# Kernel tuning notes

Measured on AMD Instinct MI355X. Metric: run time of the kernel, lower is better.

Reference implementation:

```python
import jax, jax.numpy as jnp
import numpy as np

ALPHA = 0.1
NUM_CLASSES = 10000
FEAT_DIM = 256
BATCH = 8192


def setup_inputs() -> dict:
    key = jax.random.key(0)
    k1, k2, k3 = jax.random.split(key, 3)
    feat = jax.random.normal(k1, (BATCH, FEAT_DIM), dtype=jnp.float32)
    label = jax.random.randint(k2, (BATCH,), 0, NUM_CLASSES, dtype=jnp.int64)
    # centers parameter, initialized ~ randn as in the torch constructor
    centers = jax.random.normal(k3, (NUM_CLASSES, FEAT_DIM), dtype=jnp.float32)
    return {"feat": feat, "label": label, "centers": centers}


def reference(feat, label, centers):
    B = feat.shape[0]
    # dist[b,c] = ||feat[b] - centers[c]||^2, computed in GEMM form:
    # ||f||^2 + ||c||^2 - 2 f.c  (same math as the broadcast diff^2 sum)
    f_sq = jnp.sum(feat * feat, axis=-1, keepdims=True)          # [B, 1]
    c_sq = jnp.sum(centers * centers, axis=-1)[None, :]          # [1, C]
    cross = jnp.einsum('bd,cd->bc', feat, centers)               # [B, C]
    dist = f_sq + c_sq - 2.0 * cross                             # [B, C]

    # one-hot margin scaling: y_onehot = alpha * onehot(label) + 1
    onehot = jax.nn.one_hot(label, NUM_CLASSES, dtype=dist.dtype)  # [B, C]
    margin_dist = dist * (onehot * ALPHA + 1.0)

    margin_logits = -0.5 * margin_dist
    logits = -0.5 * dist

    # likelihood: mean over batch of 0.5 * ||feat - centers[label]||^2
    cdiff = feat - centers[label]                                 # [B, D]
    likelihood = jnp.sum(cdiff * cdiff) / (2.0 * B)
    return (logits, margin_logits, likelihood)
```

## Files before the change

kernel.cpp:

```cpp
#include <hip/hip_runtime.h>
#include <hip/hip_bf16.h>


#define ALPHA_ 0.1f
constexpr int BATCH = 8192;
constexpr int NCLS  = 10000;
constexpr int FDIM  = 256;

typedef __attribute__((ext_vector_type(8))) short bf16x8;
typedef __attribute__((ext_vector_type(4))) float f32x4;

__device__ __forceinline__ unsigned short f2bf(float f) {
  unsigned int u = __float_as_uint(f);
  u += 0x7FFF + ((u >> 16) & 1);
  return (unsigned short)(u >> 16);
}

__global__ void prep_kernel(const float* __restrict__ feat,
                            const float* __restrict__ centers,
                            unsigned short* __restrict__ fbf,
                            unsigned short* __restrict__ cbf,
                            float* __restrict__ fsq,
                            float* __restrict__ csq) {
  int gw = (int)((blockIdx.x * blockDim.x + threadIdx.x) >> 6);
  int lane = threadIdx.x & 63;
  if (gw >= BATCH + NCLS) return;
  const float* src; unsigned short* dst; float* sq;
  if (gw < BATCH) {
    src = feat + (size_t)gw * FDIM; dst = fbf + (size_t)gw * FDIM; sq = fsq + gw;
  } else {
    int r = gw - BATCH;
    src = centers + (size_t)r * FDIM; dst = cbf + (size_t)r * FDIM; sq = csq + r;
  }
  float4 v = reinterpret_cast<const float4*>(src)[lane];
  ushort4 b;
  b.x = f2bf(v.x); b.y = f2bf(v.y); b.z = f2bf(v.z); b.w = f2bf(v.w);
  reinterpret_cast<ushort4*>(dst)[lane] = b;
  float s = v.x*v.x + v.y*v.y + v.z*v.z + v.w*v.w;
  #pragma unroll
  for (int off = 32; off >= 1; off >>= 1) s += __shfl_xor(s, off, 64);
  if (lane == 0) *sq = s;
}

#define BM 128
#define BN 128
#define BK 64
#define LDK 72

__global__ __launch_bounds__(512, 8)
void gemm_kernel(const unsigned short* __restrict__ fbf,
                 const unsigned short* __restrict__ cbf,
                 const float* __restrict__ fsq,
                 const float* __restrict__ csq,
                 const int* __restrict__ label,
                 float* __restrict__ out_logits,
                 float* __restrict__ out_margin) {
  __shared__ unsigned short As[BM * LDK];
  __shared__ unsigned short Bs[BN * LDK];

  const int NTN = (NCLS + BN - 1) / BN;
  const int NWG = (BATCH / BM) * NTN;

  int bid = blockIdx.x;
  int wg = (bid & 7) * (NWG >> 3) + (bid >> 3);
  int mt = wg / NTN;
  int nt = wg - mt * NTN;

  const int tid  = threadIdx.x;
  const int lane = tid & 63;
  const int wid  = tid >> 6;
  const int wr   = (wid >> 2) * 64;
  const int wc   = (wid & 3) * 32;

  f32x4 acc[4][2];
  #pragma unroll
  for (int i = 0; i < 4; i++)
    #pragma unroll
    for (int j = 0; j < 2; j++) acc[i][j] = (f32x4){0.f, 0.f, 0.f, 0.f};

  const int srow = tid >> 3;
  const int scol = (tid & 7) * 8;
  const size_t a_base = (size_t)(mt * BM) * FDIM;
  const int c0 = nt * BN;

  for (int kc = 0; kc < FDIM / BK; ++kc) {
    const int k0 = kc * BK;
    #pragma unroll
    for (int j = 0; j < 2; ++j) {
      int r = j * 64 + srow;
      bf16x8 v = *reinterpret_cast<const bf16x8*>(fbf + a_base + (size_t)r * FDIM + k0 + scol);
      *reinterpret_cast<bf16x8*>(&As[r * LDK + scol]) = v;
    }
    #pragma unroll
    for (int j = 0; j < 2; ++j) {
      int r = j * 64 + srow;
      int c = c0 + r;
      bf16x8 v = (bf16x8){0,0,0,0,0,0,0,0};
      if (c < NCLS) v = *reinterpret_cast<const bf16x8*>(cbf + (size_t)c * FDIM + k0 + scol);
      *reinterpret_cast<bf16x8*>(&Bs[r * LDK + scol]) = v;
    }
    __syncthreads();
    #pragma unroll
    for (int kk = 0; kk < BK / 32; ++kk) {
      const int kcol = kk * 32 + (lane >> 4) * 8;
      bf16x8 a[4], b[2];
      #pragma unroll
      for (int i = 0; i < 4; i++)
        a[i] = *reinterpret_cast<const bf16x8*>(&As[(wr + i * 16 + (lane & 15)) * LDK + kcol]);
      #pragma unroll
      for (int j = 0; j < 2; j++)
        b[j] = *reinterpret_cast<const bf16x8*>(&Bs[(wc + j * 16 + (lane & 15)) * LDK + kcol]);
      #pragma unroll
      for (int i = 0; i < 4; i++)
        #pragma unroll
        for (int j = 0; j < 2; j++)
          acc[i][j] = __builtin_amdgcn_mfma_f32_16x16x32_bf16(b[j], a[i], acc[i][j], 0, 0, 0);
    }
    __syncthreads();
  }

  const int mloc = wr + (lane & 15);
  const int nbase = wc + ((lane >> 4) << 2);
  #pragma unroll
  for (int i = 0; i < 4; i++) {
    int m = mt * BM + mloc + i * 16;
    float fs = fsq[m];
    int lb = label[m];
    size_t rowoff = (size_t)m * NCLS;
    #pragma unroll
    for (int j = 0; j < 2; j++) {
      int n0 = c0 + nbase + j * 16;
      if (n0 >= NCLS) continue;
      float4 cs = *reinterpret_cast<const float4*>(&csq[n0]);
      f32x4 v = acc[i][j];
      f32x4 lg;
      lg[0] = v[0] - 0.5f * (fs + cs.x);
      lg[1] = v[1] - 0.5f * (fs + cs.y);
      lg[2] = v[2] - 0.5f * (fs + cs.z);
      lg[3] = v[3] - 0.5f * (fs + cs.w);
      __builtin_nontemporal_store(lg, reinterpret_cast<f32x4*>(&out_logits[rowoff + n0]));
      f32x4 mg;
      mg[0] = (lb == n0    ) ? lg[0] * (1.0f + ALPHA_) : lg[0];
      mg[1] = (lb == n0 + 1) ? lg[1] * (1.0f + ALPHA_) : lg[1];
      mg[2] = (lb == n0 + 2) ? lg[2] * (1.0f + ALPHA_) : lg[2];
      mg[3] = (lb == n0 + 3) ? lg[3] * (1.0f + ALPHA_) : lg[3];
      __builtin_nontemporal_store(mg, reinterpret_cast<f32x4*>(&out_margin[rowoff + n0]));
    }
  }
}

__global__ void lik_partial_kernel(const float* __restrict__ feat,
                                   const int* __restrict__ label,
                                   const float* __restrict__ centers,
                                   float* __restrict__ partial) {
  int t = threadIdx.x;
  int b0 = blockIdx.x * 8;
  float acc = 0.f;
  #pragma unroll
  for (int i = 0; i < 8; i++) {
    int row = b0 + i;
    int lb = label[row];
    float d = feat[(size_t)row * FDIM + t] - centers[(size_t)lb * FDIM + t];
    acc += d * d;
  }
  #pragma unroll
  for (int off = 32; off >= 1; off >>= 1) acc += __shfl_xor(acc, off, 64);
  __shared__ float red[4];
  if ((t & 63) == 0) red[t >> 6] = acc;
  __syncthreads();
  if (t == 0) partial[blockIdx.x] = red[0] + red[1] + red[2] + red[3];
}

__global__ void lik_final_kernel(const float* __restrict__ partial,
                                 float* __restrict__ out) {
  int t = threadIdx.x;
  float v = partial[t] + partial[t + 256] + partial[t + 512] + partial[t + 768];
  #pragma unroll
  for (int off = 32; off >= 1; off >>= 1) v += __shfl_xor(v, off, 64);
  __shared__ float red[4];
  if ((t & 63) == 0) red[t >> 6] = v;
  __syncthreads();
  if (t == 0) out[0] = (red[0] + red[1] + red[2] + red[3]) * (1.0f / (2.0f * BATCH));
}

extern "C" void kernel_launch(void* const* d_in, const int* in_sizes, int n_in,
                              void* d_out, int out_size, void* d_ws, size_t ws_size,
                              hipStream_t stream) {
  const float* feat    = (const float*)d_in[0];
  const int*   label   = (const int*)d_in[1];
  const float* centers = (const float*)d_in[2];

  float* out        = (float*)d_out;
  float* out_logits = out;
  float* out_margin = out + (size_t)BATCH * NCLS;
  float* out_lik    = out + 2 * (size_t)BATCH * NCLS;

  char* ws = (char*)d_ws;
  unsigned short* fbf = (unsigned short*)ws;
  unsigned short* cbf = (unsigned short*)(ws + (size_t)BATCH * FDIM * 2);
  float* fsq     = (float*)(ws + (size_t)BATCH * FDIM * 2 + (size_t)NCLS * FDIM * 2);
  float* csq     = fsq + BATCH;
  float* partial = csq + NCLS;

  prep_kernel<<<(BATCH + NCLS) / 4, 256, 0, stream>>>(feat, centers, fbf, cbf, fsq, csq);
  lik_partial_kernel<<<BATCH / 8, 256, 0, stream>>>(feat, label, centers, partial);
  lik_final_kernel<<<1, 256, 0, stream>>>(partial, out_lik);
  gemm_kernel<<<(BATCH / BM) * ((NCLS + BN - 1) / BN), 512, 0, stream>>>(
      fbf, cbf, fsq, csq, label, out_logits, out_margin);
}
```

Measured before the change: 220.9 us.

## Double-buffer LDS tiles with register prefetch and XOR-swizzled layout in GEMM

The GEMM main loop now prefetches the next K-chunk from global memory into registers while MFMAs run on the current LDS buffer, then writes it into a second LDS buffer. This drops one barrier per iteration. Padded rows are replaced by an XOR swizzle to avoid LDS bank conflicts without the padding, and out-of-range center rows are clamped instead of zero-filled. Launch bounds drop to 4 waves per SIMD, and the double buffer doubles LDS use, which may lower occupancy in a kernel that is largely bound by output writes.

```diff
diff --git a/kernel.cpp b/kernel.cpp
--- a/kernel.cpp
+++ b/kernel.cpp
@@ -45,9 +45,8 @@
 #define BM 128
 #define BN 128
 #define BK 64
-#define LDK 72
-
-__global__ __launch_bounds__(512, 8)
+
+__global__ __launch_bounds__(512, 4)
 void gemm_kernel(const unsigned short* __restrict__ fbf,
                  const unsigned short* __restrict__ cbf,
                  const float* __restrict__ fsq,
@@ -55,8 +54,8 @@
                  const int* __restrict__ label,
                  float* __restrict__ out_logits,
                  float* __restrict__ out_margin) {
-  __shared__ unsigned short As[BM * LDK];
-  __shared__ unsigned short Bs[BN * LDK];
+  __shared__ unsigned short As[2][BM * BK];
+  __shared__ unsigned short Bs[2][BN * BK];
 
   const int NTN = (NCLS + BN - 1) / BN;
   const int NWG = (BATCH / BM) * NTN;
@@ -78,45 +77,61 @@
     #pragma unroll
     for (int j = 0; j < 2; j++) acc[i][j] = (f32x4){0.f, 0.f, 0.f, 0.f};
 
-  const int srow = tid >> 3;
-  const int scol = (tid & 7) * 8;
+  const int sr = tid >> 3;
+  const int sc = tid & 7;
   const size_t a_base = (size_t)(mt * BM) * FDIM;
   const int c0 = nt * BN;
 
+  bf16x8 va[2], vb[2];
+  #define LOADT(kc_) do {                                                      \
+    int k0 = (kc_) * BK;                                                       \
+    _Pragma("unroll")                                                          \
+    for (int j = 0; j < 2; ++j) {                                              \
+      int r = j * 64 + sr;                                                     \
+      va[j] = *reinterpret_cast<const bf16x8*>(fbf + a_base + (size_t)r * FDIM + k0 + sc * 8); \
+      int cc = c0 + r; cc = (cc < NCLS) ? cc : (NCLS - 1);                     \
+      vb[j] = *reinterpret_cast<const bf16x8*>(cbf + (size_t)cc * FDIM + k0 + sc * 8); \
+    }                                                                          \
+  } while (0)
+  #define STORET(b_) do {                                                      \
+    _Pragma("unroll")                                                          \
+    for (int j = 0; j < 2; ++j) {                                              \
+      int r = j * 64 + sr;                                                     \
+      int off = r * BK + ((sc ^ (r & 7)) * 8);                                 \
+      *reinterpret_cast<bf16x8*>(&As[b_][off]) = va[j];                        \
+      *reinterpret_cast<bf16x8*>(&Bs[b_][off]) = vb[j];                        \
+    }                                                                          \
+  } while (0)
+
+  LOADT(0);
+  STORET(0);
+
+  #pragma unroll
   for (int kc = 0; kc < FDIM / BK; ++kc) {
-    const int k0 = kc * BK;
-    #pragma unroll
-    for (int j = 0; j < 2; ++j) {
-      int r = j * 64 + srow;
-      bf16x8 v = *reinterpret_cast<const bf16x8*>(fbf + a_base + (size_t)r * FDIM + k0 + scol);
-      *reinterpret_cast<bf16x8*>(&As[r * LDK + scol]) = v;
-    }
-    #pragma unroll
-    for (int j = 0; j < 2; ++j) {
-      int r = j * 64 + srow;
-      int c = c0 + r;
-      bf16x8 v = (bf16x8){0,0,0,0,0,0,0,0};
-      if (c < NCLS) v = *reinterpret_cast<const bf16x8*>(cbf + (size_t)c * FDIM + k0 + scol);
-      *reinterpret_cast<bf16x8*>(&Bs[r * LDK + scol]) = v;
-    }
+    const int cur = kc & 1;
+    if (kc < FDIM / BK - 1) LOADT(kc + 1);
     __syncthreads();
     #pragma unroll
     for (int kk = 0; kk < BK / 32; ++kk) {
-      const int kcol = kk * 32 + (lane >> 4) * 8;
+      const int ch = kk * 4 + (lane >> 4);
       bf16x8 a[4], b[2];
       #pragma unroll
-      for (int i = 0; i < 4; i++)
-        a[i] = *reinterpret_cast<const bf16x8*>(&As[(wr + i * 16 + (lane & 15)) * LDK + kcol]);
+      for (int i = 0; i < 4; i++) {
+        int row = wr + i * 16 + (lane & 15);
+        a[i] = *reinterpret_cast<const bf16x8*>(&As[cur][row * BK + ((ch ^ (row & 7)) * 8)]);
+      }
       #pragma unroll
-      for (int j = 0; j < 2; j++)
-        b[j] = *reinterpret_cast<const bf16x8*>(&Bs[(wc + j * 16 + (lane & 15)) * LDK + kcol]);
+      for (int j = 0; j < 2; j++) {
+        int row = wc + j * 16 + (lane & 15);
+        b[j] = *reinterpret_cast<const bf16x8*>(&Bs[cur][row * BK + ((ch ^ (row & 7)) * 8)]);
+      }
       #pragma unroll
       for (int i = 0; i < 4; i++)
         #pragma unroll
         for (int j = 0; j < 2; j++)
           acc[i][j] = __builtin_amdgcn_mfma_f32_16x16x32_bf16(b[j], a[i], acc[i][j], 0, 0, 0);
     }
-    __syncthreads();
+    if (kc < FDIM / BK - 1) STORET(cur ^ 1);
   }
 
   const int mloc = wr + (lane & 15);
@@ -147,6 +162,8 @@
       __builtin_nontemporal_store(mg, reinterpret_cast<f32x4*>(&out_margin[rowoff + n0]));
     }
   }
+  #undef LOADT
+  #undef STORET
 }
 
 __global__ void lik_partial_kernel(const float* __restrict__ feat,
```

After: 210.7 us. 1.05x faster.
